# Kernel tuning notes

Measured on AMD Instinct MI355X. Metric: run time of the kernel, lower is better.

Reference implementation:

```python
import jax, jax.numpy as jnp
import numpy as np

# Static configuration matching the selected code path:
#   mode='inject_subject', is_self_attn=True, layer_id='up_blocks.0' (inject layer, bank hit)
#   alpha = AlphaScheduler.alpha(step=20, total=50, 'up_blocks.0') = 0.8 * 0.6 = 0.48
B, L, D, H = 4, 1024, 1280, 20
DH = D // H  # 64
ALPHA = 0.48


def setup_inputs() -> dict:
    key = jax.random.key(0)
    ks = jax.random.split(key, 8)
    w = lambda k, shp: (jax.random.normal(k, shp, dtype=jnp.float32) * 0.02)
    return {
        "hidden_states": jax.random.normal(ks[0], (B, L, D), dtype=jnp.float32),
        "Wq": w(ks[1], (D, D)),
        "Wk": w(ks[2], (D, D)),
        "Wv": w(ks[3], (D, D)),
        "Wo": w(ks[4], (D, D)),
        "bo": jnp.zeros((D,), dtype=jnp.float32),
        # cached background K/V, stored after head_to_batch_dim -> [B*H, L_bg, DH]
        "K_bg": jax.random.normal(ks[5], (B * H, L, DH), dtype=jnp.float32),
        "V_bg": jax.random.normal(ks[6], (B * H, L, DH), dtype=jnp.float32),
    }


def _head_to_batch(x):  # [B, L, D] -> [B*H, L, DH]
    b, l, _ = x.shape
    return x.reshape(b, l, H, DH).transpose(0, 2, 1, 3).reshape(b * H, l, DH)


def _batch_to_head(x):  # [B*H, L, DH] -> [B, L, D]
    bh, l, _ = x.shape
    b = bh // H
    return x.reshape(b, H, l, DH).transpose(0, 2, 1, 3).reshape(b, l, D)


def reference(hidden_states, Wq, Wk, Wv, Wo, bo, K_bg, V_bg):
    # q/k/v projections (self-attention: k, v from hidden_states)
    q = _head_to_batch(hidden_states @ Wq)  # [B*H, L, DH]
    k = _head_to_batch(hidden_states @ Wk)
    v = _head_to_batch(hidden_states @ Wv)

    # inject_subject: concat cached background K/V scaled by alpha along kv-seq dim
    k = jnp.concatenate([k, ALPHA * K_bg], axis=1)  # [B*H, 2L, DH]
    v = jnp.concatenate([v, ALPHA * V_bg], axis=1)

    # _sdpa: q scaled by scale*sqrt(dh), SDPA divides by sqrt(dh) -> net factor `scale`
    scale = 1.0 / jnp.sqrt(jnp.asarray(DH, dtype=q.dtype))
    scores = jnp.einsum('bqd,bkd->bqk', q, k) * scale  # [B*H, L, 2L]
    probs = jax.nn.softmax(scores, axis=-1)
    context = jnp.einsum('bqk,bkd->bqd', probs, v)  # [B*H, L, DH]

    out = _batch_to_head(context) @ Wo + bo  # to_out[0] linear
    return out
```

## Files before the change

### kernel.cpp

```cpp
#include <hip/hip_runtime.h>
#include <hip/hip_bf16.h>

#define B_   4
#define L_   1024
#define D_   1280
#define H_   20
#define DH_  64
#define BH_  (B_*H_)
#define L2_  (2*L_)
#define ALPHA_ 0.48f

typedef __attribute__((ext_vector_type(8))) short short8;
typedef __attribute__((ext_vector_type(4))) float float4v;

__device__ __forceinline__ float bf2f(ushort u) {
    union { unsigned int i; float f; } v; v.i = ((unsigned int)u) << 16; return v.f;
}
__device__ __forceinline__ ushort f2bf(float f) {
    union { float f; unsigned int i; } v; v.f = f;
    unsigned int i = v.i;
    unsigned int r = i + 0x7FFF + ((i >> 16) & 1);
    return (ushort)(r >> 16);
}
__device__ __forceinline__ short8 pack8(float4 f0, float4 f1) {
    short8 o;
    o[0] = (short)f2bf(f0.x); o[1] = (short)f2bf(f0.y);
    o[2] = (short)f2bf(f0.z); o[3] = (short)f2bf(f0.w);
    o[4] = (short)f2bf(f1.x); o[5] = (short)f2bf(f1.y);
    o[6] = (short)f2bf(f1.z); o[7] = (short)f2bf(f1.w);
    return o;
}
__device__ __forceinline__ void pack4_store(ushort* dst, float a, float b, float c, float d) {
    union { __hip_bfloat162 h; unsigned int u; } x, y;
    x.h = __float22bfloat162_rn(make_float2(a, b));
    y.h = __float22bfloat162_rn(make_float2(c, d));
    uint2 v; v.x = x.u; v.y = y.u;
    *(uint2*)dst = v;
}

__device__ __forceinline__ void async16(const void* g, void* l) {
    __builtin_amdgcn_global_load_lds(
        (__attribute__((address_space(1))) void*)g,
        (__attribute__((address_space(3))) void*)l, 16, 0, 0);
}

__global__ __launch_bounds__(256) void detect_dtype(const unsigned int* __restrict__ w,
                                                    int* __restrict__ flag) {
    __shared__ int cnt;
    if (threadIdx.x == 0) cnt = 0;
    __syncthreads();
    int local = 0;
    for (int i = threadIdx.x; i < 4096; i += 256) {
        unsigned e = (w[i] >> 7) & 0xFF;
        local += (e >= 100 && e <= 130) ? 1 : 0;
    }
    atomicAdd(&cnt, local);
    __syncthreads();
    if (threadIdx.x == 0) flag[0] = (cnt > 2048) ? 1 : 0;
}

__global__ __launch_bounds__(256) void prep(
    const void* __restrict__ w0, const void* __restrict__ w1,
    const void* __restrict__ w2, const void* __restrict__ w3,
    ushort* __restrict__ Wt,
    const void* __restrict__ Vbg, ushort* __restrict__ Vt,
    const void* __restrict__ X, ushort* __restrict__ Xb,
    const void* __restrict__ Kbg, ushort* __restrict__ Kcv,
    const int* __restrict__ flag) {
    bool is16 = flag[0] != 0;
    int bi = blockIdx.x, tid = threadIdx.x;
    if (bi < 2880) {
        bool doScale = (bi >= 1600);
        const void* src; ushort* dst; int srcld, dstld; long sbase, dbase;
        if (bi < 1600) {
            int z = bi / 400, t4 = bi % 400;
            int by = t4 / 20, bx = t4 % 20;
            const void* srcs[4] = {w0, w1, w2, w3};
            src = srcs[z]; srcld = D_; dstld = D_;
            sbase = (long)(by * 64) * D_ + bx * 64;
            dst = Wt + (long)z * D_ * D_;
            dbase = (long)(bx * 64) * D_ + by * 64;
        } else {
            int j = bi - 1600;
            int bh = j >> 4, kt = j & 15;
            src = Vbg; srcld = DH_; dstld = L2_;
            sbase = ((long)bh * L_ + kt * 64) * DH_;
            dst = Vt;
            dbase = (long)bh * DH_ * L2_ + L_ + kt * 64;
        }
        __shared__ ushort t[64 * 72];
        int ldr = tid >> 3, ldc = (tid & 7) * 8;
#pragma unroll
        for (int i = 0; i < 2; i++) {
            int y = ldr + 32 * i;
            long idx = sbase + (long)y * srcld + ldc;
            short8 v;
            if (is16) {
                v = *(const short8*)((const ushort*)src + idx);
                if (doScale) {
#pragma unroll
                    for (int j2 = 0; j2 < 8; j2++)
                        v[j2] = (short)f2bf(ALPHA_ * bf2f((ushort)v[j2]));
                }
            } else {
                const float* s = (const float*)src;
                float4 f0 = *(const float4*)&s[idx];
                float4 f1 = *(const float4*)&s[idx + 4];
                if (doScale) {
                    f0.x *= ALPHA_; f0.y *= ALPHA_; f0.z *= ALPHA_; f0.w *= ALPHA_;
                    f1.x *= ALPHA_; f1.y *= ALPHA_; f1.z *= ALPHA_; f1.w *= ALPHA_;
                }
                v = pack8(f0, f1);
            }
            *(short8*)&t[y * 72 + ldc] = v;
        }
        __syncthreads();
        int c = tid & 63, r0 = (tid >> 6) * 16;
#pragma unroll
        for (int i = 0; i < 2; i++) {
            short8 o;
#pragma unroll
            for (int j2 = 0; j2 < 8; j2++) o[j2] = (short)t[(r0 + i * 8 + j2) * 72 + c];
            *(short8*)&dst[dbase + (long)c * dstld + r0 + i * 8] = o;
        }
    } else if (bi < 5440) {
        if (is16) return;
        long i = ((long)(bi - 2880) * 256 + tid) * 8;
        const float* s = (const float*)X;
        *(short8*)&Xb[i] = pack8(*(const float4*)&s[i], *(const float4*)&s[i + 4]);
    } else {
        if (is16) return;
        long i = ((long)(bi - 5440) * 256 + tid) * 8;
        const float* s = (const float*)Kbg;
        *(short8*)&Kcv[i] = pack8(*(const float4*)&s[i], *(const float4*)&s[i + 4]);
    }
}

template<int BMt, int BNt, int WROWS, int WCOLS>
__global__ __launch_bounds__(256) void gemm_tpl(
    const ushort* __restrict__ A16, const void* __restrict__ Araw,
    const ushort* __restrict__ Bt,
    ushort* __restrict__ Qp, ushort* __restrict__ Kp, ushort* __restrict__ Vt,
    void* __restrict__ Out, const void* __restrict__ bo, int mode,
    const int* __restrict__ flag) {
    constexpr int MI = BMt / WROWS / 16;
    constexpr int NI = BNt / WCOLS / 16;
    constexpr int ASZ = BMt * 32, BSZ = BNt * 32;
    __shared__ __align__(16) ushort Al[2 * ASZ];
    __shared__ __align__(16) ushort Bl[2 * BSZ];
    bool is16 = flag[0] != 0;
    const ushort* A = (mode == 0 && is16) ? (const ushort*)Araw : A16;
    int tid = threadIdx.x;
    int bx = blockIdx.x, by = blockIdx.y;
    int w = tid >> 6, lane = tid & 63, l15 = lane & 15, quad = lane >> 4;
    int wm = (w / WCOLS) * (BMt / WROWS);
    int wn = (w % WCOLS) * (BNt / WCOLS);
    float4v acc[MI][NI] = {};
    const int K = 1280;
    constexpr int NK = 40;
    const ushort* Arow = A + (long)by * BMt * K + (tid >> 2) * K + (tid & 3) * 8;
    const ushort* Brow = Bt + (long)bx * BNt * K + (tid >> 2) * K + (tid & 3) * 8;

    auto stage = [&](int ki, int b) {
#pragma unroll
        for (int i = 0; i < BMt / 64; i++)
            async16(Arow + (long)i * 64 * K + ki * 32, &Al[b * ASZ + (i * 4 + w) * 512]);
#pragma unroll
        for (int i = 0; i < BNt / 64; i++)
            async16(Brow + (long)i * 64 * K + ki * 32, &Bl[b * BSZ + (i * 4 + w) * 512]);
    };

    stage(0, 0);
    __syncthreads();
    for (int ki = 0; ki < NK; ki++) {
        int cur = ki & 1;
        if (ki + 1 < NK) stage(ki + 1, 1 - cur);
        short8 av[MI], bv[NI];
#pragma unroll
        for (int mi = 0; mi < MI; mi++)
            av[mi] = *(const short8*)&Al[cur * ASZ + (wm + mi * 16 + l15) * 32 + quad * 8];
#pragma unroll
        for (int ni = 0; ni < NI; ni++)
            bv[ni] = *(const short8*)&Bl[cur * BSZ + (wn + ni * 16 + l15) * 32 + quad * 8];
#pragma unroll
        for (int mi = 0; mi < MI; mi++)
#pragma unroll
            for (int ni = 0; ni < NI; ni++)
                acc[mi][ni] = __builtin_amdgcn_mfma_f32_16x16x32_bf16(av[mi], bv[ni], acc[mi][ni], 0, 0, 0);
        __syncthreads();
    }

    if (mode == 0) {
        int which = bx / 10;
#pragma unroll
        for (int mi = 0; mi < MI; mi++) {
            int m0 = by * BMt + wm + mi * 16 + quad * 4;
            int b = m0 >> 10, l0 = m0 & 1023;
#pragma unroll
            for (int ni = 0; ni < NI; ni++) {
                int n = bx * BNt + wn + ni * 16 + l15;
                int np = n - which * 1280;
                int h = np >> 6, dh = np & 63;
                if (which == 0) {
#pragma unroll
                    for (int r = 0; r < 4; r++)
                        Qp[((long)(b * H_ + h) * L_ + l0 + r) * DH_ + dh] =
                            f2bf(acc[mi][ni][r] * 0.125f);
                } else if (which == 1) {
#pragma unroll
                    for (int r = 0; r < 4; r++)
                        Kp[((long)(b * H_ + h) * L_ + l0 + r) * DH_ + dh] =
                            f2bf(acc[mi][ni][r]);
                } else {
                    pack4_store(&Vt[((long)(b * H_ + h) * DH_ + dh) * L2_ + l0],
                                acc[mi][ni][0], acc[mi][ni][1],
                                acc[mi][ni][2], acc[mi][ni][3]);
                }
            }
        }
    } else {
#pragma unroll
        for (int mi = 0; mi < MI; mi++) {
            int mloc = wm + mi * 16 + quad * 4;
#pragma unroll
            for (int ni = 0; ni < NI; ni++) {
                int nloc = wn + ni * 16 + l15;
#pragma unroll
                for (int r = 0; r < 4; r++) {
                    int m = by * BMt + mloc + r;
                    int n = bx * BNt + nloc;
                    float bias = is16 ? bf2f(((const ushort*)bo)[n]) : ((const float*)bo)[n];
                    float o = acc[mi][ni][r] + bias;
                    if (is16) ((ushort*)Out)[(long)m * D_ + n] = f2bf(o);
                    else      ((float*)Out)[(long)m * D_ + n] = o;
                }
            }
        }
    }
}

#define FS 72

__global__ __launch_bounds__(256) void flash_attn(
    const ushort* __restrict__ Qp, const ushort* __restrict__ Kp,
    const void* __restrict__ KbgRaw, const ushort* __restrict__ Kcv,
    const ushort* __restrict__ Vt, ushort* __restrict__ Ctx,
    const int* __restrict__ flag) {
    __shared__ __align__(16) ushort Kl[2 * 4096], Vl[2 * 4096];
    __shared__ __align__(16) ushort Pl[128 * FS];
    const ushort* Kbg = flag[0] ? (const ushort*)KbgRaw : Kcv;
    int tid = threadIdx.x;
    int w = tid >> 6, lane = tid & 63, l15 = lane & 15, quad = lane >> 4;
    int bi = blockIdx.x;
    int bh = (bi & 7) * 10 + ((bi >> 3) % 10);
    int qt = bi / 80;

    short8 aq[2][2];
    const ushort* Qb = Qp + ((long)bh * L_ + qt * 128 + w * 32) * DH_;
#pragma unroll
    for (int mi = 0; mi < 2; mi++)
#pragma unroll
        for (int ks = 0; ks < 2; ks++)
            aq[mi][ks] = *(const short8*)&Qb[(mi * 16 + l15) * DH_ + ks * 32 + quad * 8];

    float rs[2] = {0.f, 0.f};
    float4v O[2][4] = {};
    const ushort* Vb = Vt + (long)bh * DH_ * L2_;
    int prow = (w * 32 + l15) * FS;

    auto stage = [&](int kt, int b) {
        const ushort* Ksrc = (kt < 16)
            ? Kp  + ((long)bh * L_ + kt * 64) * DH_
            : Kbg + ((long)bh * L_ + (kt - 16) * 64) * DH_;
#pragma unroll
        for (int i = 0; i < 2; i++) {
            int q = i * 4 + w;
            async16(&Ksrc[(long)lane * DH_ + q * 8], &Kl[b * 4096 + q * 512]);
            async16(&Vb[(long)lane * L2_ + kt * 64 + q * 8], &Vl[b * 4096 + q * 512]);
        }
    };

    stage(0, 0);
    __syncthreads();
    for (int kt = 0; kt < 32; kt++) {
        int cur = kt & 1;
        if (kt + 1 < 32) stage(kt + 1, 1 - cur);
        bool bg = (kt >= 16);
        short8 bk[2][4];
#pragma unroll
        for (int ks = 0; ks < 2; ks++)
#pragma unroll
            for (int nt = 0; nt < 4; nt++)
                bk[ks][nt] = *(const short8*)&Kl[cur * 4096 + (ks * 4 + quad) * 512 + (nt * 16 + l15) * 8];
#pragma unroll
        for (int mi = 0; mi < 2; mi++) {
            float4v s[4] = {};
#pragma unroll
            for (int ks = 0; ks < 2; ks++)
#pragma unroll
                for (int nt = 0; nt < 4; nt++)
                    s[nt] = __builtin_amdgcn_mfma_f32_16x16x32_bf16(bk[ks][nt], aq[mi][ks], s[nt], 0, 0, 0);
#pragma unroll
            for (int nt = 0; nt < 4; nt++) {
                float p[4];
#pragma unroll
                for (int r = 0; r < 4; r++) {
                    float sv = s[nt][r];
                    if (bg) sv *= ALPHA_;
                    p[r] = __expf(sv);
                    rs[mi] += p[r];
                }
                pack4_store(&Pl[prow + mi * 16 * FS + nt * 16 + quad * 4],
                            p[0], p[1], p[2], p[3]);
            }
        }
        short8 bv[2][4];
#pragma unroll
        for (int ks = 0; ks < 2; ks++)
#pragma unroll
            for (int nt = 0; nt < 4; nt++)
                bv[ks][nt] = *(const short8*)&Vl[cur * 4096 + (ks * 4 + quad) * 512 + (nt * 16 + l15) * 8];
        asm volatile("s_waitcnt lgkmcnt(0)\n" ::: "memory");
#pragma unroll
        for (int mi = 0; mi < 2; mi++)
#pragma unroll
            for (int ks = 0; ks < 2; ks++) {
                short8 ap = *(const short8*)&Pl[prow + mi * 16 * FS + ks * 32 + quad * 8];
#pragma unroll
                for (int nt = 0; nt < 4; nt++)
                    O[mi][nt] = __builtin_amdgcn_mfma_f32_16x16x32_bf16(bv[ks][nt], ap, O[mi][nt], 0, 0, 0);
            }
        __syncthreads();
    }
    float rcp[2];
#pragma unroll
    for (int mi = 0; mi < 2; mi++) {
        float v = rs[mi];
        v += __shfl_xor(v, 16);
        v += __shfl_xor(v, 32);
        rcp[mi] = 1.f / v;
    }
    int b = bh / H_, h = bh % H_;
#pragma unroll
    for (int mi = 0; mi < 2; mi++) {
        long l = qt * 128 + w * 32 + mi * 16 + l15;
#pragma unroll
        for (int nt = 0; nt < 4; nt++)
            pack4_store(&Ctx[(long)(b * L_ + l) * D_ + h * DH_ + nt * 16 + quad * 4],
                        O[mi][nt][0] * rcp[mi], O[mi][nt][1] * rcp[mi],
                        O[mi][nt][2] * rcp[mi], O[mi][nt][3] * rcp[mi]);
    }
}

extern "C" void kernel_launch(void* const* d_in, const int* in_sizes, int n_in,
                              void* d_out, int out_size, void* d_ws, size_t ws_size,
                              hipStream_t stream) {
    const void* X   = d_in[0];
    const void* Wq  = d_in[1];
    const void* Wk  = d_in[2];
    const void* Wv  = d_in[3];
    const void* Wo  = d_in[4];
    const void* bo  = d_in[5];
    const void* Kbg = d_in[6];
    const void* Vbg = d_in[7];

    char* ws = (char*)d_ws;
    size_t off = 0;
    auto alloc = [&](size_t bytes) {
        void* p = ws + off;
        off = (off + bytes + 255) & ~(size_t)255;
        return p;
    };
    int*    dflag = (int*)alloc(256);
    ushort* Wt    = (ushort*)alloc((size_t)4 * D_ * D_ * 2);
    ushort* Qp    = (ushort*)alloc((size_t)BH_ * L_ * DH_ * 2);
    ushort* Kp    = (ushort*)alloc((size_t)BH_ * L_ * DH_ * 2);
    ushort* Kcv   = (ushort*)alloc((size_t)BH_ * L_ * DH_ * 2);
    ushort* Vt    = (ushort*)alloc((size_t)BH_ * DH_ * L2_ * 2);
    ushort* Xb    = (ushort*)alloc((size_t)B_ * L_ * D_ * 2);
    ushort* Ctx   = Xb;
    ushort* Wqkv_t = Wt;
    ushort* Wo_t   = Wt + (size_t)3 * D_ * D_;

    dim3 tb(256);
    detect_dtype<<<1, tb, 0, stream>>>((const unsigned int*)Wq, dflag);
    prep<<<8000, tb, 0, stream>>>(Wq, Wk, Wv, Wo, Wt, Vbg, Vt, X, Xb, Kbg, Kcv, dflag);
    gemm_tpl<128, 128, 2, 2><<<dim3(30, 32), tb, 0, stream>>>(
        Xb, X, Wqkv_t, Qp, Kp, Vt, nullptr, nullptr, 0, dflag);
    flash_attn<<<dim3(640), tb, 0, stream>>>(Qp, Kp, Kbg, Kcv, Vt, Ctx, dflag);
    gemm_tpl<64, 128, 1, 4><<<dim3(10, 64), tb, 0, stream>>>(
        Ctx, nullptr, Wo_t, nullptr, nullptr, nullptr, d_out, bo, 1, dflag);
}
```

Before: 332.4 us.

## Split attention KV range across waves and fold log2e into Q scale

Restructures flash attention so each block handles 64 query rows and each of its four waves processes a disjoint quarter of the 2L keys, with per-wave private LDS buffers and no block barriers inside the loop. Partial outputs and row sums are reduced through shared memory at the end. The Q scale now includes log2(e), so the kernel can use the native exp2 instead of __expf. The aim is to remove per-iteration __syncthreads and raise parallelism (1280 blocks). The costs are a final cross-wave reduction, larger LDS use per block, and a loop that stages one redundant wrapped tile on its last iteration.

```diff
diff --git a/kernel.cpp b/kernel.cpp
--- a/kernel.cpp
+++ b/kernel.cpp
@@ -9,9 +9,16 @@
 #define BH_  (B_*H_)
 #define L2_  (2*L_)
 #define ALPHA_ 0.48f
+#define QSCALE_ 0.180336880f
 
 typedef __attribute__((ext_vector_type(8))) short short8;
 typedef __attribute__((ext_vector_type(4))) float float4v;
+
+#if __has_builtin(__builtin_amdgcn_exp2f)
+#define EXP2(x) __builtin_amdgcn_exp2f(x)
+#else
+#define EXP2(x) exp2f(x)
+#endif
 
 __device__ __forceinline__ float bf2f(ushort u) {
     union { unsigned int i; float f; } v; v.i = ((unsigned int)u) << 16; return v.f;
@@ -205,7 +212,7 @@
 #pragma unroll
                     for (int r = 0; r < 4; r++)
                         Qp[((long)(b * H_ + h) * L_ + l0 + r) * DH_ + dh] =
-                            f2bf(acc[mi][ni][r] * 0.125f);
+                            f2bf(acc[mi][ni][r] * QSCALE_);
                 } else if (which == 1) {
 #pragma unroll
                     for (int r = 0; r < 4; r++)
@@ -239,116 +246,131 @@
     }
 }
 
-#define FS 72
-
 __global__ __launch_bounds__(256) void flash_attn(
     const ushort* __restrict__ Qp, const ushort* __restrict__ Kp,
     const void* __restrict__ KbgRaw, const ushort* __restrict__ Kcv,
     const ushort* __restrict__ Vt, ushort* __restrict__ Ctx,
     const int* __restrict__ flag) {
-    __shared__ __align__(16) ushort Kl[2 * 4096], Vl[2 * 4096];
-    __shared__ __align__(16) ushort Pl[128 * FS];
+    __shared__ __align__(16) char SH[53248];
+    ushort* sh16 = (ushort*)SH;
     const ushort* Kbg = flag[0] ? (const ushort*)KbgRaw : Kcv;
     int tid = threadIdx.x;
     int w = tid >> 6, lane = tid & 63, l15 = lane & 15, quad = lane >> 4;
     int bi = blockIdx.x;
-    int bh = (bi & 7) * 10 + ((bi >> 3) % 10);
-    int qt = bi / 80;
-
-    short8 aq[2][2];
-    const ushort* Qb = Qp + ((long)bh * L_ + qt * 128 + w * 32) * DH_;
-#pragma unroll
-    for (int mi = 0; mi < 2; mi++)
+    int c = bi & 7, j = bi >> 3;
+    int bh = c * 10 + j % 10;
+    int qt = j / 10;
+
+    ushort* Kw = sh16 + w * 2048;
+    ushort* Vw = sh16 + 8192 + w * 2048;
+    ushort* Pw = sh16 + 16384 + w * 2560;
+
+    for (int i = lane; i < 1280; i += 64) ((unsigned int*)Pw)[i] = 0;
+
+    short8 aq[4][2];
+    const ushort* Qb = Qp + ((long)bh * L_ + qt * 64) * DH_;
+#pragma unroll
+    for (int mi = 0; mi < 4; mi++)
 #pragma unroll
         for (int ks = 0; ks < 2; ks++)
             aq[mi][ks] = *(const short8*)&Qb[(mi * 16 + l15) * DH_ + ks * 32 + quad * 8];
 
-    float rs[2] = {0.f, 0.f};
-    float4v O[2][4] = {};
-    const ushort* Vb = Vt + (long)bh * DH_ * L2_;
-    int prow = (w * 32 + l15) * FS;
-
-    auto stage = [&](int kt, int b) {
-        const ushort* Ksrc = (kt < 16)
-            ? Kp  + ((long)bh * L_ + kt * 64) * DH_
-            : Kbg + ((long)bh * L_ + (kt - 16) * 64) * DH_;
-#pragma unroll
-        for (int i = 0; i < 2; i++) {
-            int q = i * 4 + w;
-            async16(&Ksrc[(long)lane * DH_ + q * 8], &Kl[b * 4096 + q * 512]);
-            async16(&Vb[(long)lane * L2_ + kt * 64 + q * 8], &Vl[b * 4096 + q * 512]);
+    bool bg = (w >= 2);
+    const ushort* Ksw = bg ? Kbg + ((long)bh * L_ + (w - 2) * 512) * DH_
+                           : Kp  + ((long)bh * L_ + w * 512) * DH_;
+    const ushort* Vsw = Vt + (long)bh * DH_ * L2_ + w * 512;
+    int kvr = lane & 15, koct = lane >> 4;
+
+    auto stage = [&](int it, int buf) {
+#pragma unroll
+        for (int kc = 0; kc < 2; kc++) {
+            async16(&Ksw[(long)(it * 16 + kvr) * DH_ + kc * 32 + koct * 8],
+                    &Kw[buf * 1024 + kc * 512]);
+            async16(&Vsw[(long)lane * L2_ + it * 16 + kc * 8],
+                    &Vw[buf * 1024 + kc * 512]);
         }
     };
 
+    float rs[4] = {};
+    float4v O[4][4] = {};
+
     stage(0, 0);
-    __syncthreads();
-    for (int kt = 0; kt < 32; kt++) {
-        int cur = kt & 1;
-        if (kt + 1 < 32) stage(kt + 1, 1 - cur);
-        bool bg = (kt >= 16);
-        short8 bk[2][4];
+    for (int it = 0; it < 32; it++) {
+        int cur = it & 1;
+        stage((it + 1) & 31, 1 - cur);
+        asm volatile("s_waitcnt vmcnt(4)" ::: "memory");
+        short8 bk[2];
 #pragma unroll
         for (int ks = 0; ks < 2; ks++)
+            bk[ks] = *(const short8*)&Kw[cur * 1024 + (ks * 4 + quad) * 128 + l15 * 8];
+#pragma unroll
+        for (int mi = 0; mi < 4; mi++) {
+            float4v s = {};
+            s = __builtin_amdgcn_mfma_f32_16x16x32_bf16(bk[0], aq[mi][0], s, 0, 0, 0);
+            s = __builtin_amdgcn_mfma_f32_16x16x32_bf16(bk[1], aq[mi][1], s, 0, 0, 0);
+            float p[4];
+#pragma unroll
+            for (int r = 0; r < 4; r++) {
+                float sv = s[r];
+                if (bg) sv *= ALPHA_;
+                p[r] = EXP2(sv);
+                rs[mi] += p[r];
+            }
+            pack4_store(&Pw[mi * 640 + l15 * 40 + quad * 4], p[0], p[1], p[2], p[3]);
+        }
+        short8 bv[4];
+#pragma unroll
+        for (int nt = 0; nt < 4; nt++)
+            bv[nt] = *(const short8*)&Vw[cur * 1024 + (quad & 1) * 512 + (nt * 16 + l15) * 8];
+        asm volatile("s_waitcnt lgkmcnt(0)" ::: "memory");
+#pragma unroll
+        for (int mi = 0; mi < 4; mi++) {
+            short8 ap = *(const short8*)&Pw[mi * 640 + l15 * 40 + quad * 8];
 #pragma unroll
             for (int nt = 0; nt < 4; nt++)
-                bk[ks][nt] = *(const short8*)&Kl[cur * 4096 + (ks * 4 + quad) * 512 + (nt * 16 + l15) * 8];
-#pragma unroll
-        for (int mi = 0; mi < 2; mi++) {
-            float4v s[4] = {};
-#pragma unroll
-            for (int ks = 0; ks < 2; ks++)
-#pragma unroll
-                for (int nt = 0; nt < 4; nt++)
-                    s[nt] = __builtin_amdgcn_mfma_f32_16x16x32_bf16(bk[ks][nt], aq[mi][ks], s[nt], 0, 0, 0);
-#pragma unroll
-            for (int nt = 0; nt < 4; nt++) {
-                float p[4];
-#pragma unroll
-                for (int r = 0; r < 4; r++) {
-                    float sv = s[nt][r];
-                    if (bg) sv *= ALPHA_;
-                    p[r] = __expf(sv);
-                    rs[mi] += p[r];
-                }
-                pack4_store(&Pl[prow + mi * 16 * FS + nt * 16 + quad * 4],
-                            p[0], p[1], p[2], p[3]);
-            }
-        }
-        short8 bv[2][4];
-#pragma unroll
-        for (int ks = 0; ks < 2; ks++)
-#pragma unroll
-            for (int nt = 0; nt < 4; nt++)
-                bv[ks][nt] = *(const short8*)&Vl[cur * 4096 + (ks * 4 + quad) * 512 + (nt * 16 + l15) * 8];
-        asm volatile("s_waitcnt lgkmcnt(0)\n" ::: "memory");
-#pragma unroll
-        for (int mi = 0; mi < 2; mi++)
-#pragma unroll
-            for (int ks = 0; ks < 2; ks++) {
-                short8 ap = *(const short8*)&Pl[prow + mi * 16 * FS + ks * 32 + quad * 8];
-#pragma unroll
-                for (int nt = 0; nt < 4; nt++)
-                    O[mi][nt] = __builtin_amdgcn_mfma_f32_16x16x32_bf16(bv[ks][nt], ap, O[mi][nt], 0, 0, 0);
-            }
-        __syncthreads();
-    }
-    float rcp[2];
-#pragma unroll
-    for (int mi = 0; mi < 2; mi++) {
+                O[mi][nt] = __builtin_amdgcn_mfma_f32_16x16x32_bf16(bv[nt], ap, O[mi][nt], 0, 0, 0);
+        }
+    }
+#pragma unroll
+    for (int mi = 0; mi < 4; mi++) {
         float v = rs[mi];
         v += __shfl_xor(v, 16);
         v += __shfl_xor(v, 32);
-        rcp[mi] = 1.f / v;
-    }
-    int b = bh / H_, h = bh % H_;
-#pragma unroll
-    for (int mi = 0; mi < 2; mi++) {
-        long l = qt * 128 + w * 32 + mi * 16 + l15;
-#pragma unroll
-        for (int nt = 0; nt < 4; nt++)
-            pack4_store(&Ctx[(long)(b * L_ + l) * D_ + h * DH_ + nt * 16 + quad * 4],
-                        O[mi][nt][0] * rcp[mi], O[mi][nt][1] * rcp[mi],
-                        O[mi][nt][2] * rcp[mi], O[mi][nt][3] * rcp[mi]);
+        rs[mi] = v;
+    }
+    __syncthreads();
+    if (w > 0) {
+        float* Od = (float*)SH + (w - 1) * 4096;
+#pragma unroll
+        for (int mi = 0; mi < 4; mi++)
+#pragma unroll
+            for (int nt = 0; nt < 4; nt++)
+                *(float4v*)&Od[(mi * 4 + nt) * 256 + lane * 4] = O[mi][nt];
+        float* Rd = (float*)(SH + 49152) + (w - 1) * 64;
+        if (quad == 0) {
+#pragma unroll
+            for (int mi = 0; mi < 4; mi++) Rd[mi * 16 + l15] = rs[mi];
+        }
+    }
+    __syncthreads();
+    if (w == 0) {
+        float* Rd = (float*)(SH + 49152);
+        int b = bh / H_, h = bh % H_;
+#pragma unroll
+        for (int mi = 0; mi < 4; mi++) {
+            float tot = rs[mi] + Rd[mi * 16 + l15] + Rd[64 + mi * 16 + l15] + Rd[128 + mi * 16 + l15];
+            float rcp = 1.f / tot;
+            long l = (long)qt * 64 + mi * 16 + l15;
+#pragma unroll
+            for (int nt = 0; nt < 4; nt++) {
+                float4v o = O[mi][nt];
+#pragma unroll
+                for (int ww = 0; ww < 3; ww++)
+                    o += *(const float4v*)&((const float*)SH)[ww * 4096 + (mi * 4 + nt) * 256 + lane * 4];
+                pack4_store(&Ctx[(long)(b * L_ + l) * D_ + h * DH_ + nt * 16 + quad * 4],
+                            o[0] * rcp, o[1] * rcp, o[2] * rcp, o[3] * rcp);
+            }
+        }
     }
 }
 
@@ -387,7 +409,7 @@
     prep<<<8000, tb, 0, stream>>>(Wq, Wk, Wv, Wo, Wt, Vbg, Vt, X, Xb, Kbg, Kcv, dflag);
     gemm_tpl<128, 128, 2, 2><<<dim3(30, 32), tb, 0, stream>>>(
         Xb, X, Wqkv_t, Qp, Kp, Vt, nullptr, nullptr, 0, dflag);
-    flash_attn<<<dim3(640), tb, 0, stream>>>(Qp, Kp, Kbg, Kcv, Vt, Ctx, dflag);
+    flash_attn<<<dim3(1280), tb, 0, stream>>>(Qp, Kp, Kbg, Kcv, Vt, Ctx, dflag);
     gemm_tpl<64, 128, 1, 4><<<dim3(10, 64), tb, 0, stream>>>(
         Ctx, nullptr, Wo_t, nullptr, nullptr, nullptr, d_out, bo, 1, dflag);
 }
```

Measured after the change: 354.8 us. 1.07x slower.
